# Optimization experiments

Hardware: AMD Instinct MI355X
Metric: run time of the kernel (lower is better)

The kernel has to match this reference:

```python
import jax, jax.numpy as jnp
import numpy as np

N_SRC = 100_000   # hetero[s].num_nodes
N_DST = 100_000   # hetero[d].num_nodes
E     = 800_000   # edge_index.size(1)
D_SRC = 256       # node_dims['src']
D_DST = 256       # node_dims['dst']
D_REL = 128       # d_rel


def setup_inputs() -> dict:
    key = jax.random.key(0)
    ks = jax.random.split(key, 6)
    x_src = jax.random.normal(ks[0], (N_SRC, D_SRC), jnp.float32)
    x_dst = jax.random.normal(ks[1], (N_DST, D_DST), jnp.float32)
    # nn.Linear(d_in, d_rel, bias=False) weights, stored transposed as [d_in, d_rel]
    W_src = jax.random.normal(ks[2], (D_SRC, D_REL), jnp.float32) / np.sqrt(D_SRC).astype(np.float32)
    W_dst = jax.random.normal(ks[3], (D_DST, D_REL), jnp.float32) / np.sqrt(D_DST).astype(np.float32)
    edge_src = jax.random.randint(ks[4], (E,), 0, N_SRC, jnp.int32)  # edge_index[0]
    edge_dst = jax.random.randint(ks[5], (E,), 0, N_DST, jnp.int32)  # edge_index[1]
    return {"x_src": x_src, "x_dst": x_dst, "W_src": W_src, "W_dst": W_dst,
            "edge_src": edge_src, "edge_dst": edge_dst}


def reference(x_src, x_dst, W_src, W_dst, edge_src, edge_dst):
    # Per-type linear projection (bias-free), as in self.proj[nt](feats)
    p_src = x_src @ W_src            # [N_src, d_rel]
    p_dst = x_dst @ W_dst            # projected per module, unused by this edge type
    del p_dst

    # Degree of each destination (A.sum(dim=1)), clamped to >= 1.
    deg = jax.ops.segment_sum(jnp.ones((E,), jnp.float32), edge_dst,
                              num_segments=N_DST)
    deg = jnp.maximum(deg, 1.0)      # [N_dst]

    # Degree-normalized SpMM: sum of source features per destination / deg.
    # (coalescing duplicate edges sums their unit values; segment_sum matches.)
    agg = jax.ops.segment_sum(p_src[edge_src], edge_dst,
                              num_segments=N_DST)            # [N_dst, d_rel]
    dst = agg / deg[:, None]

    # rel_embs[et] = {'dst': dst, 'src_in': x_proj[s], 'deg_dst': deg}
    return dst, p_src, deg
```

## Files before the change

### kernel.cpp

```cpp
#include <hip/hip_runtime.h>
#include <hip/hip_bf16.h>

#define D_SRC 256
#define D_REL 128

typedef __bf16 bf16x8 __attribute__((ext_vector_type(8)));
typedef float f32x4 __attribute__((ext_vector_type(4)));

typedef const __attribute__((address_space(1))) void GASV;
typedef __attribute__((address_space(3))) void LASV;

__global__ void zero_kernel(int* __restrict__ p, int n) {
    int i = blockIdx.x * 256 + threadIdx.x;
    if (i < n) p[i] = 0;
}

__global__ __launch_bounds__(64) void prep_w_kernel(const float* __restrict__ W,
                                                    bf16x8* __restrict__ Wt) {
    int c = blockIdx.x;
    int ks = c >> 3, n = c & 7;
    int lane = threadIdx.x;
    int col = n * 16 + (lane & 15);
    int k0 = ks * 32 + (lane >> 4) * 8;
    bf16x8 v;
#pragma unroll
    for (int j = 0; j < 8; ++j) v[j] = (__bf16)W[(size_t)(k0 + j) * D_REL + col];
    Wt[c * 64 + lane] = v;
}

__global__ __launch_bounds__(256, 4) void proj_mfma_kernel(
    const float* __restrict__ x, const f32x4* __restrict__ Wt,
    float* __restrict__ out, unsigned short* __restrict__ out_bf, int M) {
    __shared__ float xlds[32 * 256];
    int tid = threadIdx.x;
    int wid = tid >> 6, lane = tid & 63;
    int r = lane & 15, kq = lane >> 4;
    int row0 = blockIdx.x * 32;

#pragma unroll
    for (int j = 0; j < 8; ++j) {
        int rl = wid * 8 + j;
        int grow = min(row0 + rl, M - 1);
        const float* src = x + (size_t)grow * D_SRC + ((lane ^ j) << 2);
        __builtin_amdgcn_global_load_lds((GASV*)src, (LASV*)&xlds[rl * 256], 16, 0, 0);
    }

    f32x4 wfv[2][8];
#pragma unroll
    for (int s = 0; s < 2; ++s)
#pragma unroll
        for (int ks = 0; ks < 8; ++ks)
            wfv[s][ks] = Wt[(ks * 8 + wid * 2 + s) * 64 + lane];
#pragma unroll
    for (int s = 0; s < 2; ++s)
#pragma unroll
        for (int ks = 0; ks < 8; ++ks)
            asm volatile("" : "+v"(wfv[s][ks]));

    __syncthreads();

    f32x4 acc[2][2];
#pragma unroll
    for (int t = 0; t < 2; ++t)
#pragma unroll
        for (int s = 0; s < 2; ++s) acc[t][s] = (f32x4)(0.f);

    const f32x4* xl = (const f32x4*)xlds;
    int r8 = r & 7;
#pragma unroll
    for (int ks = 0; ks < 8; ++ks) {
        int q0 = ks * 8 + kq * 2;
#pragma unroll
        for (int t = 0; t < 2; ++t) {
            int rl = t * 16 + r;
            f32x4 a0 = xl[rl * 64 + (q0 ^ r8)];
            f32x4 a1 = xl[rl * 64 + ((q0 + 1) ^ r8)];
            bf16x8 xf;
            xf[0] = (__bf16)a0[0]; xf[1] = (__bf16)a0[1];
            xf[2] = (__bf16)a0[2]; xf[3] = (__bf16)a0[3];
            xf[4] = (__bf16)a1[0]; xf[5] = (__bf16)a1[1];
            xf[6] = (__bf16)a1[2]; xf[7] = (__bf16)a1[3];
            acc[t][0] = __builtin_amdgcn_mfma_f32_16x16x32_bf16(
                __builtin_bit_cast(bf16x8, wfv[0][ks]), xf, acc[t][0], 0, 0, 0);
            acc[t][1] = __builtin_amdgcn_mfma_f32_16x16x32_bf16(
                __builtin_bit_cast(bf16x8, wfv[1][ks]), xf, acc[t][1], 0, 0, 0);
        }
    }

    int col0 = wid * 32;
#pragma unroll
    for (int t = 0; t < 2; ++t) {
        int prow = row0 + t * 16 + r;
        if (prow < M) {
            size_t o0 = (size_t)prow * D_REL + col0 + kq * 4;
            *(f32x4*)(out + o0) = acc[t][0];
            *(f32x4*)(out + o0 + 16) = acc[t][1];
            ushort4 b0, b1;
            b0.x = __bfloat16_as_ushort(__float2bfloat16(acc[t][0][0]));
            b0.y = __bfloat16_as_ushort(__float2bfloat16(acc[t][0][1]));
            b0.z = __bfloat16_as_ushort(__float2bfloat16(acc[t][0][2]));
            b0.w = __bfloat16_as_ushort(__float2bfloat16(acc[t][0][3]));
            b1.x = __bfloat16_as_ushort(__float2bfloat16(acc[t][1][0]));
            b1.y = __bfloat16_as_ushort(__float2bfloat16(acc[t][1][1]));
            b1.z = __bfloat16_as_ushort(__float2bfloat16(acc[t][1][2]));
            b1.w = __bfloat16_as_ushort(__float2bfloat16(acc[t][1][3]));
            *(ushort4*)(out_bf + o0) = b0;
            *(ushort4*)(out_bf + o0 + 16) = b1;
        }
    }
}

__global__ void count_kernel(const int* __restrict__ edge_dst, int* __restrict__ deg_i,
                             int* __restrict__ pos_arr, int E) {
    int e = blockIdx.x * 256 + threadIdx.x;
    if (e < E) pos_arr[e] = atomicAdd(&deg_i[edge_dst[e]], 1);
}

__global__ __launch_bounds__(1024) void scan_blocks(
    const int* __restrict__ deg_i, int* __restrict__ incl,
    int* __restrict__ bsums, int n) {
    int i = blockIdx.x * 1024 + threadIdx.x;
    int v = (i < n) ? deg_i[i] : 0;
    int lane = threadIdx.x & 63;
    int wid = threadIdx.x >> 6;
    int x = v;
#pragma unroll
    for (int off = 1; off < 64; off <<= 1) {
        int y = __shfl_up(x, off, 64);
        if (lane >= off) x += y;
    }
    __shared__ int wsum[16];
    if (lane == 63) wsum[wid] = x;
    __syncthreads();
    if (wid == 0 && lane < 16) {
        int s = wsum[lane];
#pragma unroll
        for (int off = 1; off < 16; off <<= 1) {
            int y = __shfl_up(s, off, 64);
            if (lane >= off) s += y;
        }
        wsum[lane] = s;
    }
    __syncthreads();
    int add = (wid > 0) ? wsum[wid - 1] : 0;
    x += add;
    if (i < n) incl[i] = x;
    if (threadIdx.x == 1023) bsums[blockIdx.x] = x;
}

__global__ __launch_bounds__(128) void scan_sums(int* __restrict__ bs, int nb) {
    __shared__ int tmp[128];
    int t = threadIdx.x;
    int v = (t < nb) ? bs[t] : 0;
    tmp[t] = v;
    __syncthreads();
    for (int off = 1; off < 128; off <<= 1) {
        int y = 0;
        if (t >= off) y = tmp[t - off];
        __syncthreads();
        tmp[t] += y;
        __syncthreads();
    }
    if (t < nb) bs[t] = tmp[t] - v;
}

__global__ __launch_bounds__(1024) void finalize_kernel(
    const int* __restrict__ deg_i, const int* __restrict__ incl,
    const int* __restrict__ bsums, int* __restrict__ row_start,
    float* __restrict__ deg_out, int n, int E) {
    int i = blockIdx.x * 1024 + threadIdx.x;
    if (i < n) {
        int off = bsums[blockIdx.x];
        row_start[i] = off + incl[i] - deg_i[i];
        deg_out[i] = (float)max(deg_i[i], 1);
    }
    if (i == 0) row_start[n] = E;
}

__global__ void fill_kernel(const int* __restrict__ edge_src,
                            const int* __restrict__ edge_dst,
                            const int* __restrict__ row_start,
                            const int* __restrict__ pos_arr,
                            int* __restrict__ bucket, int E) {
    int e = blockIdx.x * 256 + threadIdx.x;
    if (e < E) {
        int d = edge_dst[e];
        bucket[row_start[d] + pos_arr[e]] = edge_src[e];
    }
}

__global__ __launch_bounds__(256) void gather_kernel(
    const unsigned int* __restrict__ p_bf, const int* __restrict__ row_start,
    const int* __restrict__ bucket, const float* __restrict__ deg_out,
    float* __restrict__ dst, int n) {
    int row = blockIdx.x * 4 + (threadIdx.x >> 6);
    int lane = threadIdx.x & 63;
    if (row >= n) return;
    int beg = row_start[row], end = row_start[row + 1];
    float ax = 0.f, ay = 0.f;
    int idx = beg;
    for (; idx + 4 <= end; idx += 4) {
        int s0 = bucket[idx + 0];
        int s1 = bucket[idx + 1];
        int s2 = bucket[idx + 2];
        int s3 = bucket[idx + 3];
        unsigned int v0 = p_bf[(size_t)s0 * 64 + lane];
        unsigned int v1 = p_bf[(size_t)s1 * 64 + lane];
        unsigned int v2 = p_bf[(size_t)s2 * 64 + lane];
        unsigned int v3 = p_bf[(size_t)s3 * 64 + lane];
        ax += __uint_as_float(v0 << 16) + __uint_as_float(v1 << 16)
            + __uint_as_float(v2 << 16) + __uint_as_float(v3 << 16);
        ay += __uint_as_float(v0 & 0xffff0000u) + __uint_as_float(v1 & 0xffff0000u)
            + __uint_as_float(v2 & 0xffff0000u) + __uint_as_float(v3 & 0xffff0000u);
    }
    for (; idx < end; ++idx) {
        int s = bucket[idx];
        unsigned int v = p_bf[(size_t)s * 64 + lane];
        ax += __uint_as_float(v << 16);
        ay += __uint_as_float(v & 0xffff0000u);
    }
    float dinv = 1.0f / deg_out[row];
    float2 o;
    o.x = ax * dinv;
    o.y = ay * dinv;
    ((float2*)dst)[(size_t)row * 64 + lane] = o;
}

extern "C" void kernel_launch(void* const* d_in, const int* in_sizes, int n_in,
                              void* d_out, int out_size, void* d_ws, size_t ws_size,
                              hipStream_t stream) {
    const float* x_src = (const float*)d_in[0];
    const float* W_src = (const float*)d_in[2];
    const int* edge_src = (const int*)d_in[4];
    const int* edge_dst = (const int*)d_in[5];

    const int N_SRC = in_sizes[0] / D_SRC;
    const int N_DST = in_sizes[1] / D_SRC;
    const int E = in_sizes[4];

    float* out_dst = (float*)d_out;
    float* out_psrc = out_dst + (size_t)N_DST * D_REL;
    float* out_deg = out_psrc + (size_t)N_SRC * D_REL;

    int* deg_i = (int*)d_ws;
    int* incl = deg_i + N_DST;
    int* row_start = incl + N_DST;
    int* bsums = row_start + N_DST + 1;
    int* pos_arr = bsums + 128;
    int* bucket = pos_arr + E;
    size_t int_bytes = (size_t)(3 * N_DST + 1 + 128 + 2 * (size_t)E) * sizeof(int);
    size_t wt_off = (int_bytes + 255) & ~(size_t)255;
    bf16x8* Wt = (bf16x8*)((char*)d_ws + wt_off);
    size_t pbf_off = wt_off + 65536;
    unsigned short* p_bf = (unsigned short*)((char*)d_ws + pbf_off);

    zero_kernel<<<(N_DST + 255) / 256, 256, 0, stream>>>(deg_i, N_DST);
    prep_w_kernel<<<64, 64, 0, stream>>>(W_src, Wt);
    proj_mfma_kernel<<<(N_SRC + 31) / 32, 256, 0, stream>>>(
        x_src, (const f32x4*)Wt, out_psrc, p_bf, N_SRC);
    count_kernel<<<(E + 255) / 256, 256, 0, stream>>>(edge_dst, deg_i, pos_arr, E);
    int nb = (N_DST + 1023) / 1024;
    scan_blocks<<<nb, 1024, 0, stream>>>(deg_i, incl, bsums, N_DST);
    scan_sums<<<1, 128, 0, stream>>>(bsums, nb);
    finalize_kernel<<<nb, 1024, 0, stream>>>(deg_i, incl, bsums, row_start, out_deg, N_DST, E);
    fill_kernel<<<(E + 255) / 256, 256, 0, stream>>>(edge_src, edge_dst, row_start, pos_arr, bucket, E);
    gather_kernel<<<(N_DST + 3) / 4, 256, 0, stream>>>(
        (const unsigned int*)p_bf, row_start, bucket, out_deg, out_dst, N_DST);
}
```

Baseline: 146.5 us.

## Make projection kernel persistent with double-buffered LDS prefetch; unroll gather by eight

The projection kernel becomes persistent with 512 blocks. Each block loops over 32-row groups and prefetches the next group into a second LDS buffer while computing the current one, which amortizes the W fragment loads and hides global-load latency. The gather loop gains an 8-way unrolled path so more independent loads are in flight, and the zeroing kernel is replaced by hipMemsetAsync. In exchange, doubling LDS lowers occupancy to two blocks per CU, and the vmcnt(8) wait assumes the output stores are counted the way the code expects.

New measurement: 141.3 us. 1.04x faster.

```diff
diff --git a/kernel.cpp b/kernel.cpp
--- a/kernel.cpp
+++ b/kernel.cpp
@@ -9,11 +9,6 @@
 
 typedef const __attribute__((address_space(1))) void GASV;
 typedef __attribute__((address_space(3))) void LASV;
-
-__global__ void zero_kernel(int* __restrict__ p, int n) {
-    int i = blockIdx.x * 256 + threadIdx.x;
-    if (i < n) p[i] = 0;
-}
 
 __global__ __launch_bounds__(64) void prep_w_kernel(const float* __restrict__ W,
                                                     bf16x8* __restrict__ Wt) {
@@ -28,22 +23,26 @@
     Wt[c * 64 + lane] = v;
 }
 
-__global__ __launch_bounds__(256, 4) void proj_mfma_kernel(
+__global__ __launch_bounds__(256, 2) void proj_mfma_kernel(
     const float* __restrict__ x, const f32x4* __restrict__ Wt,
-    float* __restrict__ out, unsigned short* __restrict__ out_bf, int M) {
-    __shared__ float xlds[32 * 256];
+    float* __restrict__ out, unsigned short* __restrict__ out_bf,
+    int M, int ngroups, int nblocks) {
+    __shared__ float xlds[2][32 * 256];
     int tid = threadIdx.x;
     int wid = tid >> 6, lane = tid & 63;
     int r = lane & 15, kq = lane >> 4;
-    int row0 = blockIdx.x * 32;
-
-#pragma unroll
-    for (int j = 0; j < 8; ++j) {
-        int rl = wid * 8 + j;
-        int grow = min(row0 + rl, M - 1);
-        const float* src = x + (size_t)grow * D_SRC + ((lane ^ j) << 2);
-        __builtin_amdgcn_global_load_lds((GASV*)src, (LASV*)&xlds[rl * 256], 16, 0, 0);
-    }
+    int r8 = r & 7;
+
+    auto stagef = [&](int buf, int g) {
+        int base = g * 32;
+#pragma unroll
+        for (int j = 0; j < 8; ++j) {
+            int rl = wid * 8 + j;
+            int grow = min(base + rl, M - 1);
+            const float* src = x + (size_t)grow * D_SRC + ((lane ^ j) << 2);
+            __builtin_amdgcn_global_load_lds((GASV*)src, (LASV*)&xlds[buf][rl * 256], 16, 0, 0);
+        }
+    };
 
     f32x4 wfv[2][8];
 #pragma unroll
@@ -57,56 +56,68 @@
         for (int ks = 0; ks < 8; ++ks)
             asm volatile("" : "+v"(wfv[s][ks]));
 
-    __syncthreads();
-
-    f32x4 acc[2][2];
-#pragma unroll
-    for (int t = 0; t < 2; ++t)
-#pragma unroll
-        for (int s = 0; s < 2; ++s) acc[t][s] = (f32x4)(0.f);
-
-    const f32x4* xl = (const f32x4*)xlds;
-    int r8 = r & 7;
-#pragma unroll
-    for (int ks = 0; ks < 8; ++ks) {
-        int q0 = ks * 8 + kq * 2;
+    int g0 = blockIdx.x;
+    if (g0 < ngroups) stagef(0, g0);
+    asm volatile("s_waitcnt vmcnt(0)" ::: "memory");
+    __builtin_amdgcn_s_barrier();
+
+    int cur = 0;
+    for (int g = g0; g < ngroups; g += nblocks) {
+        int gn = g + nblocks;
+        if (gn < ngroups) stagef(cur ^ 1, gn);
+
+        f32x4 acc[2][2];
+#pragma unroll
+        for (int t = 0; t < 2; ++t)
+#pragma unroll
+            for (int s = 0; s < 2; ++s) acc[t][s] = (f32x4)(0.f);
+
+        const f32x4* xl = (const f32x4*)&xlds[cur][0];
+#pragma unroll
+        for (int ks = 0; ks < 8; ++ks) {
+            int q0 = ks * 8 + kq * 2;
+#pragma unroll
+            for (int t = 0; t < 2; ++t) {
+                int rl = t * 16 + r;
+                f32x4 a0 = xl[rl * 64 + (q0 ^ r8)];
+                f32x4 a1 = xl[rl * 64 + ((q0 + 1) ^ r8)];
+                bf16x8 xf;
+                xf[0] = (__bf16)a0[0]; xf[1] = (__bf16)a0[1];
+                xf[2] = (__bf16)a0[2]; xf[3] = (__bf16)a0[3];
+                xf[4] = (__bf16)a1[0]; xf[5] = (__bf16)a1[1];
+                xf[6] = (__bf16)a1[2]; xf[7] = (__bf16)a1[3];
+                acc[t][0] = __builtin_amdgcn_mfma_f32_16x16x32_bf16(
+                    __builtin_bit_cast(bf16x8, wfv[0][ks]), xf, acc[t][0], 0, 0, 0);
+                acc[t][1] = __builtin_amdgcn_mfma_f32_16x16x32_bf16(
+                    __builtin_bit_cast(bf16x8, wfv[1][ks]), xf, acc[t][1], 0, 0, 0);
+            }
+        }
+
+        int col0 = wid * 32;
 #pragma unroll
         for (int t = 0; t < 2; ++t) {
-            int rl = t * 16 + r;
-            f32x4 a0 = xl[rl * 64 + (q0 ^ r8)];
-            f32x4 a1 = xl[rl * 64 + ((q0 + 1) ^ r8)];
-            bf16x8 xf;
-            xf[0] = (__bf16)a0[0]; xf[1] = (__bf16)a0[1];
-            xf[2] = (__bf16)a0[2]; xf[3] = (__bf16)a0[3];
-            xf[4] = (__bf16)a1[0]; xf[5] = (__bf16)a1[1];
-            xf[6] = (__bf16)a1[2]; xf[7] = (__bf16)a1[3];
-            acc[t][0] = __builtin_amdgcn_mfma_f32_16x16x32_bf16(
-                __builtin_bit_cast(bf16x8, wfv[0][ks]), xf, acc[t][0], 0, 0, 0);
-            acc[t][1] = __builtin_amdgcn_mfma_f32_16x16x32_bf16(
-                __builtin_bit_cast(bf16x8, wfv[1][ks]), xf, acc[t][1], 0, 0, 0);
-        }
-    }
-
-    int col0 = wid * 32;
-#pragma unroll
-    for (int t = 0; t < 2; ++t) {
-        int prow = row0 + t * 16 + r;
-        if (prow < M) {
-            size_t o0 = (size_t)prow * D_REL + col0 + kq * 4;
-            *(f32x4*)(out + o0) = acc[t][0];
-            *(f32x4*)(out + o0 + 16) = acc[t][1];
-            ushort4 b0, b1;
-            b0.x = __bfloat16_as_ushort(__float2bfloat16(acc[t][0][0]));
-            b0.y = __bfloat16_as_ushort(__float2bfloat16(acc[t][0][1]));
-            b0.z = __bfloat16_as_ushort(__float2bfloat16(acc[t][0][2]));
-            b0.w = __bfloat16_as_ushort(__float2bfloat16(acc[t][0][3]));
-            b1.x = __bfloat16_as_ushort(__float2bfloat16(acc[t][1][0]));
-            b1.y = __bfloat16_as_ushort(__float2bfloat16(acc[t][1][1]));
-            b1.z = __bfloat16_as_ushort(__float2bfloat16(acc[t][1][2]));
-            b1.w = __bfloat16_as_ushort(__float2bfloat16(acc[t][1][3]));
-            *(ushort4*)(out_bf + o0) = b0;
-            *(ushort4*)(out_bf + o0 + 16) = b1;
-        }
+            int prow = g * 32 + t * 16 + r;
+            if (prow < M) {
+                size_t o0 = (size_t)prow * D_REL + col0 + kq * 4;
+                *(f32x4*)(out + o0) = acc[t][0];
+                *(f32x4*)(out + o0 + 16) = acc[t][1];
+                ushort4 b0, b1;
+                b0.x = __bfloat16_as_ushort(__float2bfloat16(acc[t][0][0]));
+                b0.y = __bfloat16_as_ushort(__float2bfloat16(acc[t][0][1]));
+                b0.z = __bfloat16_as_ushort(__float2bfloat16(acc[t][0][2]));
+                b0.w = __bfloat16_as_ushort(__float2bfloat16(acc[t][0][3]));
+                b1.x = __bfloat16_as_ushort(__float2bfloat16(acc[t][1][0]));
+                b1.y = __bfloat16_as_ushort(__float2bfloat16(acc[t][1][1]));
+                b1.z = __bfloat16_as_ushort(__float2bfloat16(acc[t][1][2]));
+                b1.w = __bfloat16_as_ushort(__float2bfloat16(acc[t][1][3]));
+                *(ushort4*)(out_bf + o0) = b0;
+                *(ushort4*)(out_bf + o0 + 16) = b1;
+            }
+        }
+
+        asm volatile("s_waitcnt vmcnt(8)" ::: "memory");
+        __builtin_amdgcn_s_barrier();
+        cur ^= 1;
     }
 }
 
@@ -199,11 +210,22 @@
     int beg = row_start[row], end = row_start[row + 1];
     float ax = 0.f, ay = 0.f;
     int idx = beg;
+    for (; idx + 8 <= end; idx += 8) {
+        int s[8];
+        unsigned int v[8];
+#pragma unroll
+        for (int u = 0; u < 8; ++u) s[u] = bucket[idx + u];
+#pragma unroll
+        for (int u = 0; u < 8; ++u) v[u] = p_bf[(size_t)s[u] * 64 + lane];
+#pragma unroll
+        for (int u = 0; u < 8; ++u) {
+            ax += __uint_as_float(v[u] << 16);
+            ay += __uint_as_float(v[u] & 0xffff0000u);
+        }
+    }
     for (; idx + 4 <= end; idx += 4) {
-        int s0 = bucket[idx + 0];
-        int s1 = bucket[idx + 1];
-        int s2 = bucket[idx + 2];
-        int s3 = bucket[idx + 3];
+        int s0 = bucket[idx + 0], s1 = bucket[idx + 1];
+        int s2 = bucket[idx + 2], s3 = bucket[idx + 3];
         unsigned int v0 = p_bf[(size_t)s0 * 64 + lane];
         unsigned int v1 = p_bf[(size_t)s1 * 64 + lane];
         unsigned int v2 = p_bf[(size_t)s2 * 64 + lane];
@@ -254,10 +276,14 @@
     size_t pbf_off = wt_off + 65536;
     unsigned short* p_bf = (unsigned short*)((char*)d_ws + pbf_off);
 
-    zero_kernel<<<(N_DST + 255) / 256, 256, 0, stream>>>(deg_i, N_DST);
+    hipMemsetAsync(deg_i, 0, (size_t)N_DST * sizeof(int), stream);
     prep_w_kernel<<<64, 64, 0, stream>>>(W_src, Wt);
-    proj_mfma_kernel<<<(N_SRC + 31) / 32, 256, 0, stream>>>(
-        x_src, (const f32x4*)Wt, out_psrc, p_bf, N_SRC);
+    {
+        int ngroups = (N_SRC + 31) / 32;
+        int nblocks = 512;
+        proj_mfma_kernel<<<nblocks, 256, 0, stream>>>(
+            x_src, (const f32x4*)Wt, out_psrc, p_bf, N_SRC, ngroups, nblocks);
+    }
     count_kernel<<<(E + 255) / 256, 256, 0, stream>>>(edge_dst, deg_i, pos_arr, E);
     int nb = (N_DST + 1023) / 1024;
     scan_blocks<<<nb, 1024, 0, stream>>>(deg_i, incl, bsums, N_DST);
```
